# Performance work log

Measured on AMD Instinct MI355X. Metric: run time of the kernel, lower is better.

The kernel has to match this reference:

```python
import jax, jax.numpy as jnp
import numpy as np

N = 8192
D = 512


def setup_inputs() -> dict:
    key = jax.random.key(0)
    ks = jax.random.split(key, 7)
    X = jax.random.normal(ks[0], (N, D), dtype=jnp.float32)
    adj = jax.random.randint(ks[1], (N, N), 0, 2, dtype=jnp.int32)
    # guarantee at least one neighbor per row (self-loop) so softmax is defined
    adj = adj.at[jnp.arange(N), jnp.arange(N)].set(1)
    s = 1.0 / np.sqrt(D)
    Wq = jax.random.normal(ks[2], (D, D), dtype=jnp.float32) * s
    Wk = jax.random.normal(ks[3], (D, D), dtype=jnp.float32) * s
    Wv = jax.random.normal(ks[4], (D, D), dtype=jnp.float32) * s
    Wo = jax.random.normal(ks[5], (D, D), dtype=jnp.float32) * s
    bo = jnp.zeros((D,), dtype=jnp.float32)
    return {"X": X, "adj": adj, "Wq": Wq, "Wk": Wk, "Wv": Wv, "Wo": Wo, "bo": bo}


def reference(X, adj, Wq, Wk, Wv, Wo, bo):
    # torch Linear(no bias): y = x @ W.T
    Q = X @ Wq.T                                  # [N, D]
    K = X @ Wk.T                                  # [N, D]
    V = X @ Wv.T                                  # [N, D]
    scale = 1.0 / jnp.sqrt(jnp.asarray(D, X.dtype))
    scores = jnp.einsum('nd,md->nm', Q, K) * scale  # [N, N]
    scores = jnp.where(adj == 0, -jnp.inf, scores)
    attn = jax.nn.softmax(scores, axis=-1)          # [N, N]
    out = attn @ V                                  # [N, D]
    out = out @ Wo.T + bo                           # [N, D]
    return out
```

## Files before the change

### kernel.cpp

```cpp
#include <hip/hip_runtime.h>

namespace {

constexpr int NR = 8192;
constexpr int DD = 512;
constexpr int NSPLIT = 4;
constexpr int KVLEN = NR / NSPLIT;
constexpr int KT = 32;
constexpr int NT = KVLEN / KT;
constexpr int QB = 64;
constexpr float SCALE = 0.04419417382415922f;
constexpr float THR = 5.0f;

typedef __bf16 bf16x8 __attribute__((ext_vector_type(8)));
typedef __bf16 bf16x4 __attribute__((ext_vector_type(4)));
typedef float  f32x16 __attribute__((ext_vector_type(16)));

__device__ __forceinline__ f32x16 mfma(bf16x8 a, bf16x8 b, f32x16 c) {
    return __builtin_amdgcn_mfma_f32_32x32x16_bf16(a, b, c, 0, 0, 0);
}

typedef const __attribute__((address_space(1))) void g_void;
typedef __attribute__((address_space(3))) void l_void;
__device__ __forceinline__ void lds_dma16(const void* g, void* l) {
    __builtin_amdgcn_global_load_lds((g_void*)g, (l_void*)l, 16, 0, 0);
}

__global__ void __launch_bounds__(256)
cast_kernel(const float* __restrict__ in, __bf16* __restrict__ out, int n8) {
    int i = blockIdx.x * 256 + threadIdx.x;
    if (i >= n8) return;
    const float4* p = (const float4*)(in + (size_t)i * 8);
    float4 v0 = p[0], v1 = p[1];
    bf16x8 o;
    o[0] = (__bf16)v0.x; o[1] = (__bf16)v0.y; o[2] = (__bf16)v0.z; o[3] = (__bf16)v0.w;
    o[4] = (__bf16)v1.x; o[5] = (__bf16)v1.y; o[6] = (__bf16)v1.z; o[7] = (__bf16)v1.w;
    *(bf16x8*)(out + (size_t)i * 8) = o;
}

template<bool FINAL>
__global__ void __launch_bounds__(256, 2)
gemm_kernel(const __bf16* __restrict__ A, const __bf16* __restrict__ B0,
            const __bf16* __restrict__ B1, const __bf16* __restrict__ B2,
            __bf16* __restrict__ C0, __bf16* __restrict__ C1, __bf16* __restrict__ C2,
            const float* __restrict__ bias, float* __restrict__ Cf)
{
    const __bf16* B = B0;
    __bf16* Cb = C0;
    if (!FINAL) {
        if (blockIdx.y == 1)      { B = B1; Cb = C1; }
        else if (blockIdx.y == 2) { B = B2; Cb = C2; }
    }
    __shared__ __bf16 As[128][72];
    __shared__ __bf16 Bs[128][72];
    const int t = threadIdx.x;
    const int w = t >> 6, lane = t & 63, lo = lane & 31, hi = lane >> 5;
    const int wm = w >> 1, wn = w & 1;
    const int bm = (blockIdx.x >> 2) * 128;
    const int bn = (blockIdx.x & 3) * 128;

    f32x16 acc[2][2];
    #pragma unroll
    for (int a = 0; a < 2; ++a)
        #pragma unroll
        for (int b = 0; b < 2; ++b)
            #pragma unroll
            for (int r = 0; r < 16; ++r) acc[a][b][r] = 0.f;

    for (int k0 = 0; k0 < DD; k0 += 64) {
        __syncthreads();
        #pragma unroll
        for (int pp = 0; pp < 2; ++pp) {
            int r = pp * 64 + (t >> 2), c = (t & 3) * 16;
            *(bf16x8*)&As[r][c]     = *(const bf16x8*)(A + (size_t)(bm + r) * DD + k0 + c);
            *(bf16x8*)&As[r][c + 8] = *(const bf16x8*)(A + (size_t)(bm + r) * DD + k0 + c + 8);
            *(bf16x8*)&Bs[r][c]     = *(const bf16x8*)(B + (size_t)(bn + r) * DD + k0 + c);
            *(bf16x8*)&Bs[r][c + 8] = *(const bf16x8*)(B + (size_t)(bn + r) * DD + k0 + c + 8);
        }
        __syncthreads();
        #pragma unroll
        for (int ks = 0; ks < 4; ++ks) {
            bf16x8 a0 = *(const bf16x8*)&As[wm * 64 + lo][ks * 16 + hi * 8];
            bf16x8 a1 = *(const bf16x8*)&As[wm * 64 + 32 + lo][ks * 16 + hi * 8];
            bf16x8 b0 = *(const bf16x8*)&Bs[wn * 64 + lo][ks * 16 + hi * 8];
            bf16x8 b1 = *(const bf16x8*)&Bs[wn * 64 + 32 + lo][ks * 16 + hi * 8];
            acc[0][0] = mfma(a0, b0, acc[0][0]);
            acc[0][1] = mfma(a0, b1, acc[0][1]);
            acc[1][0] = mfma(a1, b0, acc[1][0]);
            acc[1][1] = mfma(a1, b1, acc[1][1]);
        }
    }
    #pragma unroll
    for (int mi = 0; mi < 2; ++mi)
        #pragma unroll
        for (int ni = 0; ni < 2; ++ni) {
            int col = bn + wn * 64 + ni * 32 + lo;
            float bv = 0.f;
            if (FINAL) bv = bias[col];
            #pragma unroll
            for (int r = 0; r < 16; ++r) {
                int row = bm + wm * 64 + mi * 32 + (r & 3) + 8 * (r >> 2) + 4 * hi;
                if (FINAL) Cf[(size_t)row * DD + col] = acc[mi][ni][r] + bv;
                else       Cb[(size_t)row * DD + col] = (__bf16)acc[mi][ni][r];
            }
        }
}

__global__ void __launch_bounds__(256)
transpose_kernel(const __bf16* __restrict__ V, __bf16* __restrict__ Vt) {
    __shared__ __bf16 tile[64][72];
    const int t = threadIdx.x;
    const int rb = blockIdx.x * 64;
    const int cb = blockIdx.y * 64;
    #pragma unroll
    for (int pp = 0; pp < 2; ++pp) {
        int r = pp * 32 + (t >> 3), c = (t & 7) * 8;
        *(bf16x8*)&tile[r][c] = *(const bf16x8*)(V + (size_t)(rb + r) * DD + cb + c);
    }
    __syncthreads();
    #pragma unroll
    for (int pp = 0; pp < 2; ++pp) {
        int dd = pp * 32 + (t >> 3), co = (t & 7) * 8;
        bf16x8 o;
        #pragma unroll
        for (int j = 0; j < 8; ++j) o[j] = tile[co + j][dd];
        *(bf16x8*)(Vt + (size_t)(cb + dd) * NR + rb + co) = o;
    }
}

__global__ void __launch_bounds__(256, 1)
flash_kernel(const __bf16* __restrict__ Qg, const __bf16* __restrict__ Kg,
             const __bf16* __restrict__ Vt, const int* __restrict__ adj,
             __bf16* __restrict__ Opart, float* __restrict__ lse)
{
    __shared__ __bf16 Ksw[2][4][KT][128];
    __shared__ __bf16 Vsw[4][128][KT];
    __shared__ __bf16 Sp[4][QB][40];
    __shared__ __bf16 Pl[QB][40];
    __shared__ float  fl[QB];
    __shared__ float  ll[QB];
    __shared__ int    flg[4];

    const int t = threadIdx.x;
    const int w = t >> 6, lane = t & 63, lo = lane & 31, hi = lane >> 5;
    const int qblk = blockIdx.x * QB;
    const int split = blockIdx.y;
    const int kv0 = split * KVLEN;

    bf16x8 qa[2][8];
    #pragma unroll
    for (int mi = 0; mi < 2; ++mi)
        #pragma unroll
        for (int ks = 0; ks < 8; ++ks)
            qa[mi][ks] = *(const bf16x8*)(Qg + (size_t)(qblk + mi * 32 + lo) * DD + w * 128 + ks * 16 + hi * 8);

    f32x16 O[2][2][2];
    #pragma unroll
    for (int h = 0; h < 2; ++h)
        #pragma unroll
        for (int a = 0; a < 2; ++a)
            #pragma unroll
            for (int b = 0; b < 2; ++b)
                #pragma unroll
                for (int r = 0; r < 16; ++r) O[h][a][b][r] = 0.f;

    const int qo = w * 16 + (lane >> 2);
    const int c8 = (lane & 3) * 8;
    const int* adjp = adj + (size_t)(qblk + qo) * NR + kv0 + c8;

    const int l16 = lane & 15, lr4 = lane >> 4;
    const int l4  = lane & 3,  lr2 = lane >> 2;

    #pragma unroll
    for (int i = 0; i < 8; ++i) {
        int r = i * 4 + lr4;
        int g = l16 ^ (r & 7);
        lds_dma16(Kg + (size_t)(kv0 + r) * DD + w * 128 + g * 8, &Ksw[0][w][i * 4][0]);
    }
    int4 aA = *(const int4*)adjp;
    int4 aB = *(const int4*)(adjp + 4);

    float m_run = -1e30f, l_run = 0.f;

    for (int tl = 0; tl < NT; ++tl) {
        const int cb = tl & 1, nb = cb ^ 1;
        const int kvb = kv0 + tl * KT;
        const int tn = (tl + 1 == NT) ? 0 : tl + 1;
        const int kvn = kv0 + tn * KT;

        #pragma unroll
        for (int i = 0; i < 8; ++i) {
            int r = i * 16 + lr2;
            int g = l4 ^ ((r >> 1) & 3);
            lds_dma16(Vt + (size_t)(w * 128 + r) * NR + kvb + g * 8, &Vsw[w][i * 16][0]);
        }
        #pragma unroll
        for (int i = 0; i < 8; ++i) {
            int r = i * 4 + lr4;
            int g = l16 ^ (r & 7);
            lds_dma16(Kg + (size_t)(kvn + r) * DD + w * 128 + g * 8, &Ksw[nb][w][i * 4][0]);
        }
        int4 naA = *(const int4*)(adjp + tn * KT);
        int4 naB = *(const int4*)(adjp + tn * KT + 4);

        asm volatile("s_waitcnt vmcnt(18)" ::: "memory");

        f32x16 St0, St1;
        #pragma unroll
        for (int r = 0; r < 16; ++r) { St0[r] = 0.f; St1[r] = 0.f; }
        #pragma unroll
        for (int ks = 0; ks < 8; ++ks) {
            int cK = ((2 * ks + hi) ^ (lo & 7)) * 8;
            bf16x8 kb = *(const bf16x8*)&Ksw[cb][w][lo][cK];
            St0 = mfma(kb, qa[0][ks], St0);
            St1 = mfma(kb, qa[1][ks], St1);
        }
        #pragma unroll
        for (int g = 0; g < 4; ++g) {
            bf16x4 v0, v1;
            #pragma unroll
            for (int j = 0; j < 4; ++j) { v0[j] = (__bf16)St0[4 * g + j]; v1[j] = (__bf16)St1[4 * g + j]; }
            *(bf16x4*)&Sp[w][lo][8 * g + 4 * hi]      = v0;
            *(bf16x4*)&Sp[w][32 + lo][8 * g + 4 * hi] = v1;
        }
        asm volatile("s_waitcnt lgkmcnt(0)\n\ts_barrier" ::: "memory");

        {
            bf16x8 p0 = *(const bf16x8*)&Sp[0][qo][c8];
            bf16x8 p1 = *(const bf16x8*)&Sp[1][qo][c8];
            bf16x8 p2 = *(const bf16x8*)&Sp[2][qo][c8];
            bf16x8 p3 = *(const bf16x8*)&Sp[3][qo][c8];
            int am[8] = {aA.x, aA.y, aA.z, aA.w, aB.x, aB.y, aB.z, aB.w};
            float s[8];
            #pragma unroll
            for (int i = 0; i < 8; ++i) {
                float v = ((float)p0[i] + (float)p1[i] + (float)p2[i] + (float)p3[i]) * SCALE;
                s[i] = (am[i] != 0) ? v : -1e30f;
            }
            float mx = s[0];
            #pragma unroll
            for (int i = 1; i < 8; ++i) mx = fmaxf(mx, s[i]);
            mx = fmaxf(mx, __shfl_xor(mx, 1));
            mx = fmaxf(mx, __shfl_xor(mx, 2));
            bool need = mx > m_run + THR;
            float m_new = need ? mx : m_run;
            float f = need ? __expf(m_run - m_new) : 1.f;
            float lsum = 0.f;
            bf16x8 pb;
            #pragma unroll
            for (int i = 0; i < 8; ++i) {
                float pv = __expf(s[i] - m_new);
                lsum += pv;
                pb[i] = (__bf16)pv;
            }
            lsum += __shfl_xor(lsum, 1);
            lsum += __shfl_xor(lsum, 2);
            l_run = l_run * f + lsum;
            m_run = m_new;
            *(bf16x8*)&Pl[qo][c8] = pb;
            if ((lane & 3) == 0) fl[qo] = f;
            unsigned long long bal = __ballot(need);
            if (lane == 0) flg[w] = (bal != 0ull) ? 1 : 0;
            aA = naA; aB = naB;
        }
        asm volatile("s_waitcnt lgkmcnt(0)\n\ts_barrier" ::: "memory");

        if (flg[0] | flg[1] | flg[2] | flg[3]) {
            #pragma unroll
            for (int mi = 0; mi < 2; ++mi)
                #pragma unroll
                for (int g = 0; g < 4; ++g) {
                    float4 fv = *(const float4*)&fl[mi * 32 + 8 * g + 4 * hi];
                    #pragma unroll
                    for (int j = 0; j < 4; ++j) {
                        float fac = (&fv.x)[j];
                        #pragma unroll
                        for (int h = 0; h < 2; ++h)
                            #pragma unroll
                            for (int ni = 0; ni < 2; ++ni)
                                O[h][mi][ni][g * 4 + j] *= fac;
                    }
                }
        }
        bf16x8 pa[2][2];
        #pragma unroll
        for (int mi = 0; mi < 2; ++mi)
            #pragma unroll
            for (int ks = 0; ks < 2; ++ks)
                pa[mi][ks] = *(const bf16x8*)&Pl[mi * 32 + lo][ks * 16 + hi * 8];

        asm volatile("s_waitcnt vmcnt(8)" ::: "memory");

        #pragma unroll
        for (int h = 0; h < 2; ++h)
            #pragma unroll
            for (int ni = 0; ni < 2; ++ni) {
                const int dr = h * 64 + ni * 32 + lo;
                const int sw = (dr >> 1) & 3;
                #pragma unroll
                for (int ks = 0; ks < 2; ++ks) {
                    int cV = ((2 * ks + hi) ^ sw) * 8;
                    bf16x8 vb = *(const bf16x8*)&Vsw[w][dr][cV];
                    O[h][0][ni] = mfma(pa[0][ks], vb, O[h][0][ni]);
                    O[h][1][ni] = mfma(pa[1][ks], vb, O[h][1][ni]);
                }
            }
    }
    if ((lane & 3) == 0) {
        ll[qo] = l_run;
        lse[(size_t)split * NR + qblk + qo] = m_run + __logf(l_run);
    }
    __syncthreads();
    #pragma unroll
    for (int mi = 0; mi < 2; ++mi)
        #pragma unroll
        for (int g = 0; g < 4; ++g) {
            float4 lv = *(const float4*)&ll[mi * 32 + 8 * g + 4 * hi];
            #pragma unroll
            for (int j = 0; j < 4; ++j) {
                float inv = 1.f / (&lv.x)[j];
                int row = qblk + mi * 32 + 8 * g + 4 * hi + j;
                #pragma unroll
                for (int h = 0; h < 2; ++h)
                    #pragma unroll
                    for (int ni = 0; ni < 2; ++ni) {
                        int col = w * 128 + h * 64 + ni * 32 + lo;
                        Opart[(size_t)split * NR * DD + (size_t)row * DD + col] =
                            (__bf16)(O[h][mi][ni][g * 4 + j] * inv);
                    }
            }
        }
}

__global__ void __launch_bounds__(256)
merge_kernel(const __bf16* __restrict__ Opart, const float* __restrict__ lse,
             __bf16* __restrict__ attn)
{
    int idx = blockIdx.x * 256 + threadIdx.x;
    int q = idx >> 6;
    int c = (idx & 63) * 8;
    float l0 = lse[q], l1 = lse[NR + q], l2 = lse[2 * NR + q], l3 = lse[3 * NR + q];
    float M = fmaxf(fmaxf(l0, l1), fmaxf(l2, l3));
    float w0 = __expf(l0 - M), w1 = __expf(l1 - M), w2 = __expf(l2 - M), w3 = __expf(l3 - M);
    float Winv = 1.f / (w0 + w1 + w2 + w3);
    const size_t base = (size_t)q * DD + c;
    const size_t stride = (size_t)NR * DD;
    bf16x8 o0 = *(const bf16x8*)(Opart + base);
    bf16x8 o1 = *(const bf16x8*)(Opart + stride + base);
    bf16x8 o2 = *(const bf16x8*)(Opart + 2 * stride + base);
    bf16x8 o3 = *(const bf16x8*)(Opart + 3 * stride + base);
    bf16x8 o;
    #pragma unroll
    for (int i = 0; i < 8; ++i)
        o[i] = (__bf16)((w0 * (float)o0[i] + w1 * (float)o1[i] +
                         w2 * (float)o2[i] + w3 * (float)o3[i]) * Winv);
    *(bf16x8*)(attn + base) = o;
}

}

extern "C" void kernel_launch(void* const* d_in, const int* in_sizes, int n_in,
                              void* d_out, int out_size, void* d_ws, size_t ws_size,
                              hipStream_t stream)
{
    (void)in_sizes; (void)n_in; (void)out_size; (void)ws_size;
    const float* X  = (const float*)d_in[0];
    const int*   adj = (const int*)d_in[1];
    const float* Wq = (const float*)d_in[2];
    const float* Wk = (const float*)d_in[3];
    const float* Wv = (const float*)d_in[4];
    const float* Wo = (const float*)d_in[5];
    const float* bo = (const float*)d_in[6];
    float* out = (float*)d_out;

    char* ws = (char*)d_ws;
    __bf16* Xb   = (__bf16*)(ws + 0);
    __bf16* Att  = (__bf16*)(ws + 0);
    __bf16* Wqb  = (__bf16*)(ws + 8388608);
    __bf16* Wkb  = (__bf16*)(ws + 8912896);
    __bf16* Wvb  = (__bf16*)(ws + 9437184);
    __bf16* Wob  = (__bf16*)(ws + 9961472);
    __bf16* Qb   = (__bf16*)(ws + 10485760);
    __bf16* Kb   = (__bf16*)(ws + 18874368);
    __bf16* Vb   = (__bf16*)(ws + 27262976);
    __bf16* Vtb  = (__bf16*)(ws + 35651584);
    __bf16* Op   = (__bf16*)(ws + 44040192);
    float*  lseb = (float*)(ws + 77594624);

    cast_kernel<<<2048, 256, 0, stream>>>(X,  Xb,  NR * DD / 8);
    cast_kernel<<<128,  256, 0, stream>>>(Wq, Wqb, DD * DD / 8);
    cast_kernel<<<128,  256, 0, stream>>>(Wk, Wkb, DD * DD / 8);
    cast_kernel<<<128,  256, 0, stream>>>(Wv, Wvb, DD * DD / 8);
    cast_kernel<<<128,  256, 0, stream>>>(Wo, Wob, DD * DD / 8);

    gemm_kernel<false><<<dim3(256, 3), 256, 0, stream>>>(Xb, Wqb, Wkb, Wvb,
                                                         Qb, Kb, Vb, nullptr, nullptr);
    transpose_kernel<<<dim3(128, 8), 256, 0, stream>>>(Vb, Vtb);
    flash_kernel<<<dim3(128, NSPLIT), 256, 0, stream>>>(Qb, Kb, Vtb, adj, Op, lseb);
    merge_kernel<<<2048, 256, 0, stream>>>(Op, lseb, Att);
    gemm_kernel<true><<<dim3(256, 1), 256, 0, stream>>>(Att, Wob, nullptr, nullptr,
                                                        nullptr, nullptr, nullptr, bo, out);
}
```

Measured before the change: 527.0 us.

## Share one LDS buffer for K and V to fit two blocks per CU

Replaces the double-buffered K tiles and the separate V tile with a single per-wave KV buffer that holds K, then V, then the next K in sequence. Launch bounds are raised to allow two workgroups per CU. The aim is higher occupancy so another block can hide memory latency. In exchange, loads within a block are serialized: V is fetched only after the score MFMAs, and the next K only after the PV MFMAs, with a full vmcnt(0) wait. This removes intra-block prefetch overlap and halves the register budget, which may cause spills.

```diff
diff --git a/kernel.cpp b/kernel.cpp
--- a/kernel.cpp
+++ b/kernel.cpp
@@ -128,13 +128,12 @@
     }
 }
 
-__global__ void __launch_bounds__(256, 1)
+__global__ void __launch_bounds__(256, 2)
 flash_kernel(const __bf16* __restrict__ Qg, const __bf16* __restrict__ Kg,
              const __bf16* __restrict__ Vt, const int* __restrict__ adj,
              __bf16* __restrict__ Opart, float* __restrict__ lse)
 {
-    __shared__ __bf16 Ksw[2][4][KT][128];
-    __shared__ __bf16 Vsw[4][128][KT];
+    __shared__ __bf16 KV[4][4096];
     __shared__ __bf16 Sp[4][QB][40];
     __shared__ __bf16 Pl[QB][40];
     __shared__ float  fl[QB];
@@ -175,55 +174,46 @@
     for (int i = 0; i < 8; ++i) {
         int r = i * 4 + lr4;
         int g = l16 ^ (r & 7);
-        lds_dma16(Kg + (size_t)(kv0 + r) * DD + w * 128 + g * 8, &Ksw[0][w][i * 4][0]);
-    }
+        lds_dma16(Kg + (size_t)(kv0 + r) * DD + w * 128 + g * 8, &KV[w][i * 512]);
+    }
+    asm volatile("" ::: "memory");
     int4 aA = *(const int4*)adjp;
     int4 aB = *(const int4*)(adjp + 4);
 
     float m_run = -1e30f, l_run = 0.f;
 
     for (int tl = 0; tl < NT; ++tl) {
-        const int cb = tl & 1, nb = cb ^ 1;
         const int kvb = kv0 + tl * KT;
         const int tn = (tl + 1 == NT) ? 0 : tl + 1;
-        const int kvn = kv0 + tn * KT;
-
+
+        asm volatile("s_waitcnt vmcnt(2)" ::: "memory");
+
+        f32x16 St0, St1;
+        #pragma unroll
+        for (int r = 0; r < 16; ++r) { St0[r] = 0.f; St1[r] = 0.f; }
+        #pragma unroll
+        for (int ks = 0; ks < 8; ++ks) {
+            int cK = ((2 * ks + hi) ^ (lo & 7)) * 8;
+            bf16x8 kb = *(const bf16x8*)&KV[w][lo * 128 + cK];
+            St0 = mfma(kb, qa[0][ks], St0);
+            St1 = mfma(kb, qa[1][ks], St1);
+        }
+        #pragma unroll
+        for (int g = 0; g < 4; ++g) {
+            bf16x4 v0, v1;
+            #pragma unroll
+            for (int j = 0; j < 4; ++j) { v0[j] = (__bf16)St0[4 * g + j]; v1[j] = (__bf16)St1[4 * g + j]; }
+            *(bf16x4*)&Sp[w][lo][8 * g + 4 * hi]      = v0;
+            *(bf16x4*)&Sp[w][32 + lo][8 * g + 4 * hi] = v1;
+        }
+        asm volatile("s_waitcnt lgkmcnt(0)" ::: "memory");
         #pragma unroll
         for (int i = 0; i < 8; ++i) {
             int r = i * 16 + lr2;
             int g = l4 ^ ((r >> 1) & 3);
-            lds_dma16(Vt + (size_t)(w * 128 + r) * NR + kvb + g * 8, &Vsw[w][i * 16][0]);
-        }
-        #pragma unroll
-        for (int i = 0; i < 8; ++i) {
-            int r = i * 4 + lr4;
-            int g = l16 ^ (r & 7);
-            lds_dma16(Kg + (size_t)(kvn + r) * DD + w * 128 + g * 8, &Ksw[nb][w][i * 4][0]);
-        }
-        int4 naA = *(const int4*)(adjp + tn * KT);
-        int4 naB = *(const int4*)(adjp + tn * KT + 4);
-
-        asm volatile("s_waitcnt vmcnt(18)" ::: "memory");
-
-        f32x16 St0, St1;
-        #pragma unroll
-        for (int r = 0; r < 16; ++r) { St0[r] = 0.f; St1[r] = 0.f; }
-        #pragma unroll
-        for (int ks = 0; ks < 8; ++ks) {
-            int cK = ((2 * ks + hi) ^ (lo & 7)) * 8;
-            bf16x8 kb = *(const bf16x8*)&Ksw[cb][w][lo][cK];
-            St0 = mfma(kb, qa[0][ks], St0);
-            St1 = mfma(kb, qa[1][ks], St1);
-        }
-        #pragma unroll
-        for (int g = 0; g < 4; ++g) {
-            bf16x4 v0, v1;
-            #pragma unroll
-            for (int j = 0; j < 4; ++j) { v0[j] = (__bf16)St0[4 * g + j]; v1[j] = (__bf16)St1[4 * g + j]; }
-            *(bf16x4*)&Sp[w][lo][8 * g + 4 * hi]      = v0;
-            *(bf16x4*)&Sp[w][32 + lo][8 * g + 4 * hi] = v1;
-        }
-        asm volatile("s_waitcnt lgkmcnt(0)\n\ts_barrier" ::: "memory");
+            lds_dma16(Vt + (size_t)(w * 128 + r) * NR + kvb + g * 8, &KV[w][i * 512]);
+        }
+        asm volatile("s_barrier" ::: "memory");
 
         {
             bf16x8 p0 = *(const bf16x8*)&Sp[0][qo][c8];
@@ -261,9 +251,9 @@
             if ((lane & 3) == 0) fl[qo] = f;
             unsigned long long bal = __ballot(need);
             if (lane == 0) flg[w] = (bal != 0ull) ? 1 : 0;
-            aA = naA; aB = naB;
-        }
-        asm volatile("s_waitcnt lgkmcnt(0)\n\ts_barrier" ::: "memory");
+        }
+        asm volatile("s_waitcnt lgkmcnt(0)" ::: "memory");
+        asm volatile("s_barrier" ::: "memory");
 
         if (flg[0] | flg[1] | flg[2] | flg[3]) {
             #pragma unroll
@@ -289,7 +279,7 @@
             for (int ks = 0; ks < 2; ++ks)
                 pa[mi][ks] = *(const bf16x8*)&Pl[mi * 32 + lo][ks * 16 + hi * 8];
 
-        asm volatile("s_waitcnt vmcnt(8)" ::: "memory");
+        asm volatile("s_waitcnt vmcnt(0)" ::: "memory");
 
         #pragma unroll
         for (int h = 0; h < 2; ++h)
@@ -300,11 +290,22 @@
                 #pragma unroll
                 for (int ks = 0; ks < 2; ++ks) {
                     int cV = ((2 * ks + hi) ^ sw) * 8;
-                    bf16x8 vb = *(const bf16x8*)&Vsw[w][dr][cV];
+                    bf16x8 vb = *(const bf16x8*)&KV[w][dr * 32 + cV];
                     O[h][0][ni] = mfma(pa[0][ks], vb, O[h][0][ni]);
                     O[h][1][ni] = mfma(pa[1][ks], vb, O[h][1][ni]);
                 }
             }
+        asm volatile("s_waitcnt lgkmcnt(0)" ::: "memory");
+        #pragma unroll
+        for (int i = 0; i < 8; ++i) {
+            int r = i * 4 + lr4;
+            int g = l16 ^ (r & 7);
+            lds_dma16(Kg + (size_t)(kv0 + tn * KT + r) * DD + w * 128 + g * 8, &KV[w][i * 512]);
+        }
+        asm volatile("" ::: "memory");
+        aA = *(const int4*)(adjp + tn * KT);
+        aB = *(const int4*)(adjp + tn * KT + 4);
+        asm volatile("" ::: "memory");
     }
     if ((lane & 3) == 0) {
         ll[qo] = l_run;
```

New measurement: 541.0 us. 1.03x slower.
